# Kernel tuning notes

Hardware: AMD Instinct MI355X
Metric: run time of the kernel (lower is better)

## Reference

```python
import jax, jax.numpy as jnp
import numpy as np

NUM_ITERATIONS = 3


def squash(x, axis):
    # squared_norm/(1+squared_norm) * x / sqrt(squared_norm), as in the torch module
    sn = jnp.sum(x * x, axis=axis, keepdims=True)
    return sn / (1.0 + sn) * x / jnp.sqrt(sn)


def setup_inputs() -> dict:
    key = jax.random.key(0)
    k1, k2 = jax.random.split(key)
    batch, num_caps, num_route, in_ch, out_ch = 32, 32, 4608, 8, 16
    x = jax.random.normal(k1, (batch, num_route, in_ch), dtype=jnp.float32)
    route_weights = jax.random.normal(k2, (num_caps, num_route, in_ch, out_ch), dtype=jnp.float32)
    return {"x": x, "route_weights": route_weights}


def reference(x, route_weights):
    # U[b,c,r,1,o] = x[b,1,r,1,i] @ W[1,c,r,i,o]
    U = jnp.einsum("bri,crio->bcro", x, route_weights)[:, :, :, None, :]  # [b,c,r,1,o]
    B = jnp.zeros_like(U)
    V = None
    for _ in range(NUM_ITERATIONS):
        C = jax.nn.softmax(B, axis=1)                 # softmax over capsules
        S = jnp.sum(C * U, axis=2, keepdims=True)      # reduce over route nodes: [b,c,1,1,o]
        V = squash(S, axis=-1)
        B = B + U * V
    b, c = B.shape[0], B.shape[1]
    o = B.shape[-1]
    return V.reshape(b, c, o)
```

## Files before the change

### kernel.cpp

```cpp
#include <hip/hip_runtime.h>

#define BATCH 32
#define NCAPS 32
#define NR    4608
#define NI    8
#define NO    16
#define CSTR  200
#define MAXRB 36
#define NCH   256
#define L2E   1.44269504088896341f

typedef float f2 __attribute__((ext_vector_type(2)));
typedef _Float16 half4v __attribute__((ext_vector_type(4)));
typedef _Float16 half8v __attribute__((ext_vector_type(8)));

template<int RB>
__global__ __launch_bounds__(1024, 2) void caps_route_store(
    const float* __restrict__ x,
    const float* __restrict__ W,
    float* __restrict__ P,
    unsigned short* __restrict__ Uh)
{
    constexpr int NP = RB / 2;
    __shared__ __align__(16) float Ws[2][2][NCAPS * CSTR];
    __shared__ __align__(16) f2    xP[RB][8][2][NI];

    const int t  = threadIdx.x;
    const int om = (t & 3) | (((t >> 3) & 1) << 2);
    const int co = ((t >> 4) & 1) | (((t >> 2) & 1) << 1) | (((t >> 5) & 1) << 2);
    const int w  = t >> 6;
    const int oh = w & 1;
    const int bq = w >> 1;
    const int o  = oh * 8 + om;
    const int b0 = 4 * bq;
    const int r0 = blockIdx.x * RB;

    f2 acc[2][4];
#pragma unroll
    for (int p = 0; p < 2; ++p)
#pragma unroll
        for (int cl = 0; cl < 4; ++cl) acc[p][cl] = (f2)0.f;

    for (int s = t; s < RB * 16; s += 1024) {
        const int rr = s >> 4, bp = s & 15;
        const float* xp0 = &x[((size_t)(2 * bp + 0) * NR + r0 + rr) * NI];
        const float* xp1 = &x[((size_t)(2 * bp + 1) * NR + r0 + rr) * NI];
        const float4 a0 = *(const float4*)xp0;
        const float4 a1 = *(const float4*)(xp0 + 4);
        const float4 c0 = *(const float4*)xp1;
        const float4 c1 = *(const float4*)(xp1 + 4);
        f2* d = &xP[rr][bp >> 1][bp & 1][0];
        d[0] = f2{a0.x, c0.x}; d[1] = f2{a0.y, c0.y};
        d[2] = f2{a0.z, c0.z}; d[3] = f2{a0.w, c0.w};
        d[4] = f2{a1.x, c1.x}; d[5] = f2{a1.y, c1.y};
        d[6] = f2{a1.z, c1.z}; d[7] = f2{a1.w, c1.w};
    }

    const int c_st = t >> 5;
    const int sl   = (c_st >> 2) + 8 * (c_st & 3);
    const int part = t & 31;
    const int i_st = part >> 2;
    const int o0   = (part & 3) * 4;
    const int dst  = sl * CSTR + o0 * 12 + i_st;
    const float* wsrc = W + ((size_t)c_st * NR + r0) * (NI * NO) + part * 4;

    {
        const float4 s0 = *(const float4*)wsrc;
        const float4 s1 = *(const float4*)(wsrc + NI * NO);
        float* d0 = &Ws[0][0][dst];
        d0[0] = s0.x; d0[12] = s0.y; d0[24] = s0.z; d0[36] = s0.w;
        float* d1 = &Ws[0][1][dst];
        d1[0] = s1.x; d1[12] = s1.y; d1[24] = s1.z; d1[36] = s1.w;
    }
    float4 pfa = {}, pfb = {};
    if (NP > 1) {
        pfa = *(const float4*)(wsrc + 2 * NI * NO);
        pfb = *(const float4*)(wsrc + 3 * NI * NO);
    }
    __syncthreads();

    auto compute_store = [&](const float* wt, const f2* xv, int r) {
        f2 xq[2][NI];
#pragma unroll
        for (int i = 0; i < NI; ++i) { xq[0][i] = xv[i]; xq[1][i] = xv[NI + i]; }
        const float* wb = wt + co * CSTR + o * 12;
        f2 u[2][4];
#pragma unroll
        for (int cl = 0; cl < 4; ++cl) {
            const float* wp = wb + cl * (8 * CSTR);
            const float4 w0 = *(const float4*)wp;
            const float4 w1 = *(const float4*)(wp + 4);
#pragma unroll
            for (int p = 0; p < 2; ++p) {
                f2 u2 = xq[p][0] * w0.x;
                u2 += xq[p][1] * w0.y;
                u2 += xq[p][2] * w0.z;
                u2 += xq[p][3] * w0.w;
                u2 += xq[p][4] * w1.x;
                u2 += xq[p][5] * w1.y;
                u2 += xq[p][6] * w1.z;
                u2 += xq[p][7] * w1.w;
                u[p][cl] = u2;
                acc[p][cl] += u2;
            }
        }
        unsigned short* ub = Uh + (((size_t)r * BATCH + b0) * NO + o) * NCAPS + 4 * co;
#pragma unroll
        for (int bb = 0; bb < 4; ++bb) {
            const int p = bb >> 1, h = bb & 1;
            half4v hv;
            hv[0] = (_Float16)(h ? u[p][0].y : u[p][0].x);
            hv[1] = (_Float16)(h ? u[p][1].y : u[p][1].x);
            hv[2] = (_Float16)(h ? u[p][2].y : u[p][2].x);
            hv[3] = (_Float16)(h ? u[p][3].y : u[p][3].x);
            *(half4v*)(ub + (size_t)bb * (NO * NCAPS)) = hv;
        }
    };

#pragma unroll 1
    for (int rp = 0; rp < NP; ++rp) {
        const int cur = rp & 1;
        if (rp + 1 < NP) {
            float* d0 = &Ws[cur ^ 1][0][dst];
            d0[0] = pfa.x; d0[12] = pfa.y; d0[24] = pfa.z; d0[36] = pfa.w;
            float* d1 = &Ws[cur ^ 1][1][dst];
            d1[0] = pfb.x; d1[12] = pfb.y; d1[24] = pfb.z; d1[36] = pfb.w;
            if (rp + 2 < NP) {
                pfa = *(const float4*)(wsrc + (size_t)(2 * rp + 4) * (NI * NO));
                pfb = *(const float4*)(wsrc + (size_t)(2 * rp + 5) * (NI * NO));
            }
        }
        compute_store(&Ws[cur][0][0], &xP[2 * rp + 0][bq][0][0], r0 + 2 * rp + 0);
        compute_store(&Ws[cur][1][0], &xP[2 * rp + 1][bq][0][0], r0 + 2 * rp + 1);
        __syncthreads();
    }

#pragma unroll
    for (int bb = 0; bb < 4; ++bb) {
        const int p = bb >> 1, h = bb & 1;
        float* pout = P + (((size_t)blockIdx.x * BATCH + b0 + bb) * NO + o) * NCAPS + 4 * co;
        float4 v;
        v.x = (h ? acc[p][0].y : acc[p][0].x) * 0.03125f;
        v.y = (h ? acc[p][1].y : acc[p][1].x) * 0.03125f;
        v.z = (h ? acc[p][2].y : acc[p][2].x) * 0.03125f;
        v.w = (h ? acc[p][3].y : acc[p][3].x) * 0.03125f;
        *(float4*)pout = v;
    }
}

template<int RB>
__global__ __launch_bounds__(1024, 2) void caps_route_cached(
    const unsigned short* __restrict__ Uh,
    const float* __restrict__ A,
    float* __restrict__ P)
{
    const int t  = threadIdx.x;
    const int ch = t & 1;
    const int o  = (t >> 1) & 15;
    const int b  = t >> 5;
    const int r0 = blockIdx.x * RB;

    float a2[16];
#pragma unroll
    for (int cc = 0; cc < 16; ++cc)
        a2[cc] = A[(b * NCAPS + 16 * ch + cc) * NO + o] * L2E;
    float acc[16];
#pragma unroll
    for (int cc = 0; cc < 16; ++cc) acc[cc] = 0.f;

    const unsigned short* up =
        Uh + (((size_t)r0 * BATCH + b) * NO + o) * NCAPS + ch * 16;

#pragma unroll 1
    for (int rr = 0; rr < RB; ++rr) {
        const uint4 q0 = *(const uint4*)(up);
        const uint4 q1 = *(const uint4*)(up + 8);
        up += BATCH * NO * NCAPS;
        const half8v h0 = __builtin_bit_cast(half8v, q0);
        const half8v h1 = __builtin_bit_cast(half8v, q1);
        float u[16];
#pragma unroll
        for (int k = 0; k < 8; ++k) { u[k] = (float)h0[k]; u[8 + k] = (float)h1[k]; }
        float Z = 0.f;
        float tt[16];
#pragma unroll
        for (int cc = 0; cc < 16; ++cc) {
            const float uu = u[cc];
            const float ee = exp2f(uu * a2[cc]);
            Z += ee;
            tt[cc] = ee * uu;
        }
        Z += __shfl_xor(Z, 1);
        const float rz = __builtin_amdgcn_rcpf(Z);
#pragma unroll
        for (int cc = 0; cc < 16; ++cc)
            acc[cc] = fmaf(tt[cc], rz, acc[cc]);
    }

    float* pout = P + (((size_t)blockIdx.x * BATCH + b) * NO + o) * NCAPS + ch * 16;
#pragma unroll
    for (int q = 0; q < 4; ++q) {
        float4 v;
        v.x = acc[4 * q + 0]; v.y = acc[4 * q + 1];
        v.z = acc[4 * q + 2]; v.w = acc[4 * q + 3];
        *(float4*)(pout + 4 * q) = v;
    }
}

template<int RB, bool FIRST>
__global__ __launch_bounds__(1024, 2) void caps_route_fast(
    const float* __restrict__ x, const float* __restrict__ W,
    const float* __restrict__ A, float* __restrict__ P)
{
    constexpr int NP = RB / 2;
    __shared__ __align__(16) float Ws[2][2][NCAPS * CSTR];
    __shared__ __align__(16) f2    xP[RB][8][2][NI];

    const int t  = threadIdx.x;
    const int om = (t & 3) | (((t >> 3) & 1) << 2);
    const int co = ((t >> 4) & 1) | (((t >> 2) & 1) << 1) | (((t >> 5) & 1) << 2);
    const int w  = t >> 6;
    const int oh = w & 1;
    const int bq = w >> 1;
    const int o  = oh * 8 + om;
    const int b0 = 4 * bq;
    const int r0 = blockIdx.x * RB;

    f2 a2[2][4];
    if (!FIRST) {
#pragma unroll
        for (int p = 0; p < 2; ++p)
#pragma unroll
            for (int cl = 0; cl < 4; ++cl) {
                const int c = 4 * co + cl;
                a2[p][cl].x = A[((b0 + 2 * p + 0) * NCAPS + c) * NO + o] * L2E;
                a2[p][cl].y = A[((b0 + 2 * p + 1) * NCAPS + c) * NO + o] * L2E;
            }
    }
    f2 acc[2][4];
#pragma unroll
    for (int p = 0; p < 2; ++p)
#pragma unroll
        for (int cl = 0; cl < 4; ++cl) acc[p][cl] = (f2)0.f;

    for (int s = t; s < RB * 16; s += 1024) {
        const int rr = s >> 4, bp = s & 15;
        const float* xp0 = &x[((size_t)(2 * bp + 0) * NR + r0 + rr) * NI];
        const float* xp1 = &x[((size_t)(2 * bp + 1) * NR + r0 + rr) * NI];
        const float4 a0 = *(const float4*)xp0;
        const float4 a1 = *(const float4*)(xp0 + 4);
        const float4 c0 = *(const float4*)xp1;
        const float4 c1 = *(const float4*)(xp1 + 4);
        f2* d = &xP[rr][bp >> 1][bp & 1][0];
        d[0] = f2{a0.x, c0.x}; d[1] = f2{a0.y, c0.y};
        d[2] = f2{a0.z, c0.z}; d[3] = f2{a0.w, c0.w};
        d[4] = f2{a1.x, c1.x}; d[5] = f2{a1.y, c1.y};
        d[6] = f2{a1.z, c1.z}; d[7] = f2{a1.w, c1.w};
    }

    const int c_st = t >> 5;
    const int sl   = (c_st >> 2) + 8 * (c_st & 3);
    const int part = t & 31;
    const int i_st = part >> 2;
    const int o0   = (part & 3) * 4;
    const int dst  = sl * CSTR + o0 * 12 + i_st;
    const float* wsrc = W + ((size_t)c_st * NR + r0) * (NI * NO) + part * 4;

    {
        const float4 s0 = *(const float4*)wsrc;
        const float4 s1 = *(const float4*)(wsrc + NI * NO);
        float* d0 = &Ws[0][0][dst];
        d0[0] = s0.x; d0[12] = s0.y; d0[24] = s0.z; d0[36] = s0.w;
        float* d1 = &Ws[0][1][dst];
        d1[0] = s1.x; d1[12] = s1.y; d1[24] = s1.z; d1[36] = s1.w;
    }
    float4 pfa = {}, pfb = {};
    if (NP > 1) {
        pfa = *(const float4*)(wsrc + 2 * NI * NO);
        pfb = *(const float4*)(wsrc + 3 * NI * NO);
    }
    __syncthreads();

    auto compute_r = [&](const float* wt, const f2* xv) {
        f2 xq[2][NI];
#pragma unroll
        for (int i = 0; i < NI; ++i) { xq[0][i] = xv[i]; xq[1][i] = xv[NI + i]; }
        const float* wb = wt + co * CSTR + o * 12;
        if (FIRST) {
#pragma unroll
            for (int cl = 0; cl < 4; ++cl) {
                const float* wp = wb + cl * (8 * CSTR);
                const float4 w0 = *(const float4*)wp;
                const float4 w1 = *(const float4*)(wp + 4);
#pragma unroll
                for (int p = 0; p < 2; ++p) {
                    f2 u2 = xq[p][0] * w0.x;
                    u2 += xq[p][1] * w0.y;
                    u2 += xq[p][2] * w0.z;
                    u2 += xq[p][3] * w0.w;
                    u2 += xq[p][4] * w1.x;
                    u2 += xq[p][5] * w1.y;
                    u2 += xq[p][6] * w1.z;
                    u2 += xq[p][7] * w1.w;
                    acc[p][cl] += u2;
                }
            }
        } else {
            f2 tt[2][4];
            f2 Z0 = (f2)0.f, Z1 = (f2)0.f;
#pragma unroll
            for (int cl = 0; cl < 4; ++cl) {
                const float* wp = wb + cl * (8 * CSTR);
                const float4 w0 = *(const float4*)wp;
                const float4 w1 = *(const float4*)(wp + 4);
                f2 u0 = xq[0][0] * w0.x;
                u0 += xq[0][1] * w0.y;
                u0 += xq[0][2] * w0.z;
                u0 += xq[0][3] * w0.w;
                u0 += xq[0][4] * w1.x;
                u0 += xq[0][5] * w1.y;
                u0 += xq[0][6] * w1.z;
                u0 += xq[0][7] * w1.w;
                f2 u1 = xq[1][0] * w0.x;
                u1 += xq[1][1] * w0.y;
                u1 += xq[1][2] * w0.z;
                u1 += xq[1][3] * w0.w;
                u1 += xq[1][4] * w1.x;
                u1 += xq[1][5] * w1.y;
                u1 += xq[1][6] * w1.z;
                u1 += xq[1][7] * w1.w;
                const f2 l0 = u0 * a2[0][cl];
                const f2 l1 = u1 * a2[1][cl];
                f2 e0, e1;
                e0.x = exp2f(l0.x); e0.y = exp2f(l0.y);
                e1.x = exp2f(l1.x); e1.y = exp2f(l1.y);
                Z0 += e0; Z1 += e1;
                tt[0][cl] = e0 * u0;
                tt[1][cl] = e1 * u1;
            }
#pragma unroll
            for (int m = 0; m < 3; ++m) {
                const int msk = (m == 0) ? 4 : (m == 1) ? 16 : 32;
                Z0.x += __shfl_xor(Z0.x, msk); Z0.y += __shfl_xor(Z0.y, msk);
                Z1.x += __shfl_xor(Z1.x, msk); Z1.y += __shfl_xor(Z1.y, msk);
            }
            f2 rz0, rz1;
            rz0.x = __builtin_amdgcn_rcpf(Z0.x); rz0.y = __builtin_amdgcn_rcpf(Z0.y);
            rz1.x = __builtin_amdgcn_rcpf(Z1.x); rz1.y = __builtin_amdgcn_rcpf(Z1.y);
#pragma unroll
            for (int cl = 0; cl < 4; ++cl) {
                acc[0][cl] += tt[0][cl] * rz0;
                acc[1][cl] += tt[1][cl] * rz1;
            }
        }
    };

#pragma unroll 1
    for (int rp = 0; rp < NP; ++rp) {
        const int cur = rp & 1;
        if (rp + 1 < NP) {
            float* d0 = &Ws[cur ^ 1][0][dst];
            d0[0] = pfa.x; d0[12] = pfa.y; d0[24] = pfa.z; d0[36] = pfa.w;
            float* d1 = &Ws[cur ^ 1][1][dst];
            d1[0] = pfb.x; d1[12] = pfb.y; d1[24] = pfb.z; d1[36] = pfb.w;
            if (rp + 2 < NP) {
                pfa = *(const float4*)(wsrc + (size_t)(2 * rp + 4) * (NI * NO));
                pfb = *(const float4*)(wsrc + (size_t)(2 * rp + 5) * (NI * NO));
            }
        }
        compute_r(&Ws[cur][0][0], &xP[2 * rp + 0][bq][0][0]);
        compute_r(&Ws[cur][1][0], &xP[2 * rp + 1][bq][0][0]);
        __syncthreads();
    }

#pragma unroll
    for (int bb = 0; bb < 4; ++bb) {
        const int p = bb >> 1, h = bb & 1;
        float* pout = P + (((size_t)blockIdx.x * BATCH + b0 + bb) * NO + o) * NCAPS + 4 * co;
        float4 v;
        v.x = h ? acc[p][0].y : acc[p][0].x;
        v.y = h ? acc[p][1].y : acc[p][1].x;
        v.z = h ? acc[p][2].y : acc[p][2].x;
        v.w = h ? acc[p][3].y : acc[p][3].x;
        if (FIRST) { v.x *= 0.03125f; v.y *= 0.03125f; v.z *= 0.03125f; v.w *= 0.03125f; }
        *(float4*)pout = v;
    }
}

__global__ __launch_bounds__(256) void caps_partial(const float* __restrict__ P,
                                                    float* __restrict__ P2)
{
    const int tid = threadIdx.x;
    const int ct  = blockIdx.x & 15;
    const int rg  = blockIdx.x >> 4;
    const size_t col = (size_t)ct * 1024 + tid * 4;
    const float* p = P + (size_t)rg * 16 * 16384 + col;
    float4 s = {0.f, 0.f, 0.f, 0.f};
#pragma unroll
    for (int k = 0; k < 16; ++k) {
        const float4 v = *(const float4*)(p + (size_t)k * 16384);
        s.x += v.x; s.y += v.y; s.z += v.z; s.w += v.w;
    }
    *(float4*)(P2 + (size_t)rg * 16384 + col) = s;
}

__global__ void caps_reduce_squash(const float* __restrict__ P,
                                   float* __restrict__ A,
                                   float* __restrict__ out,
                                   int nchunk)
{
    __shared__ float sm[256];
    const int bc  = blockIdx.x;
    const int b   = bc >> 5;
    const int c   = bc & 31;
    const int tid = threadIdx.x;
    const int o = tid & 15;
    const int j = tid >> 4;
    float s = 0.f;
    for (int tch = j; tch < nchunk; tch += 16)
        s += P[(((size_t)tch * BATCH + b) * NO + o) * NCAPS + c];
    sm[tid] = s;
    __syncthreads();
    if (tid < 16) {
        float S = 0.f;
#pragma unroll
        for (int k = 0; k < 16; ++k) S += sm[tid + 16 * k];
        float sq = S * S;
#pragma unroll
        for (int d = 8; d >= 1; d >>= 1) sq += __shfl_xor(sq, d, 16);
        const float scale = sq / ((1.f + sq) * sqrtf(sq));
        const float V = S * scale;
        const int idx = bc * NO + tid;
        A[idx] += V;
        if (out) out[idx] = V;
    }
}

__global__ __launch_bounds__(512, 2) void caps_route_generic(
    const float* __restrict__ x, const float* __restrict__ W,
    const float* __restrict__ A, float* __restrict__ P, int rb)
{
    __shared__ __align__(16) float Ws[NCAPS * CSTR];
    __shared__ __align__(16) float xsT[NI * MAXRB * BATCH];

    const int t = threadIdx.x;
    const int b = t & 31;
    const int o = t >> 5;
    const int r0 = blockIdx.x * rb;
    const int rbs = rb * BATCH;

    float a2s[NCAPS];
#pragma unroll
    for (int c = 0; c < NCAPS; ++c)
        a2s[c] = A[(b * NCAPS + c) * NO + o] * L2E;
    float acc[NCAPS];
#pragma unroll
    for (int c = 0; c < NCAPS; ++c) acc[c] = 0.f;

    for (int s = t; s < rbs; s += 512) {
        const int rr = s >> 5, bb = s & 31;
        const float4 v0 = *(const float4*)&x[((size_t)bb * NR + r0 + rr) * NI];
        const float4 v1 = *(const float4*)&x[((size_t)bb * NR + r0 + rr) * NI + 4];
        const float tmp[8] = {v0.x, v0.y, v0.z, v0.w, v1.x, v1.y, v1.z, v1.w};
#pragma unroll
        for (int i = 0; i < NI; ++i) xsT[i * rbs + s] = tmp[i];
    }

    const int cs  = t >> 4;
    const int seg = t & 15;
    const int iw  = seg >> 1;
    const int ob  = (seg & 1) * 8;
    const float* wsrc = W + ((size_t)cs * NR + r0) * (NI * NO) + seg * 8;
    float4 pf0 = *(const float4*)wsrc;
    float4 pf1 = *(const float4*)(wsrc + 4);

    for (int rr = 0; rr < rb; ++rr) {
        __syncthreads();
        {
            const float tmp[8] = {pf0.x, pf0.y, pf0.z, pf0.w,
                                  pf1.x, pf1.y, pf1.z, pf1.w};
#pragma unroll
            for (int k = 0; k < 8; ++k)
                Ws[cs * CSTR + (ob + k) * 12 + iw] = tmp[k];
        }
        if (rr + 1 < rb) {
            wsrc += NI * NO;
            pf0 = *(const float4*)wsrc;
            pf1 = *(const float4*)(wsrc + 4);
        }
        __syncthreads();

        float xq[NI];
#pragma unroll
        for (int i = 0; i < NI; ++i) xq[i] = xsT[i * rbs + rr * 32 + b];

        float tt[NCAPS];
        float Z = 0.f;
        const float* bp2 = &Ws[o * 12];
#pragma unroll
        for (int c = 0; c < NCAPS; ++c) {
            const float* wp = bp2 + c * CSTR;
            const float4 w0 = *(const float4*)wp;
            const float4 w1 = *(const float4*)(wp + 4);
            float uu =      xq[0] * w0.x;
            uu = fmaf(xq[1], w0.y, uu);
            uu = fmaf(xq[2], w0.z, uu);
            uu = fmaf(xq[3], w0.w, uu);
            uu = fmaf(xq[4], w1.x, uu);
            uu = fmaf(xq[5], w1.y, uu);
            uu = fmaf(xq[6], w1.z, uu);
            uu = fmaf(xq[7], w1.w, uu);
            const float ee = exp2f(uu * a2s[c]);
            Z += ee;
            tt[c] = ee * uu;
        }
        const float rz = __builtin_amdgcn_rcpf(Z);
#pragma unroll
        for (int c = 0; c < NCAPS; ++c)
            acc[c] = fmaf(tt[c], rz, acc[c]);
    }

    float* pout = P + (((size_t)blockIdx.x * BATCH + b) * NO + o) * NCAPS;
#pragma unroll
    for (int q = 0; q < NCAPS / 4; ++q) {
        float4 v;
        v.x = acc[4 * q + 0]; v.y = acc[4 * q + 1];
        v.z = acc[4 * q + 2]; v.w = acc[4 * q + 3];
        *(float4*)(pout + 4 * q) = v;
    }
}

__global__ void caps_zero(float* __restrict__ p, int n)
{
    const int i = blockIdx.x * blockDim.x + threadIdx.x;
    if (i < n) p[i] = 0.f;
}

extern "C" void kernel_launch(void* const* d_in, const int* in_sizes, int n_in,
                              void* d_out, int out_size, void* d_ws, size_t ws_size,
                              hipStream_t stream)
{
    const float* x = (const float*)d_in[0];
    const float* W = (const float*)d_in[1];
    float* out = (float*)d_out;

    const size_t elem = (size_t)BATCH * NCAPS * NO;
    float* A  = (float*)d_ws;
    float* P  = A + elem;
    float* P2 = P + (size_t)NCH * elem;
    unsigned short* Uh = (unsigned short*)(P2 + 16 * elem);

    const size_t need_base = (size_t)(1 + NCH + 16) * elem * sizeof(float);
    const size_t need_u    = (size_t)NR * elem * sizeof(unsigned short);

    caps_zero<<<(int)((elem + 255) / 256), 256, 0, stream>>>(A, (int)elem);

    if (ws_size >= need_base + need_u) {
        caps_route_store<NR / NCH><<<NCH, 1024, 0, stream>>>(x, W, P, Uh);
        caps_partial<<<256, 256, 0, stream>>>(P, P2);
        caps_reduce_squash<<<BATCH * NCAPS, 256, 0, stream>>>(P2, A, nullptr, 16);
        caps_route_cached<NR / NCH><<<NCH, 1024, 0, stream>>>(Uh, A, P);
        caps_partial<<<256, 256, 0, stream>>>(P, P2);
        caps_reduce_squash<<<BATCH * NCAPS, 256, 0, stream>>>(P2, A, nullptr, 16);
        caps_route_cached<NR / NCH><<<NCH, 1024, 0, stream>>>(Uh, A, P);
        caps_partial<<<256, 256, 0, stream>>>(P, P2);
        caps_reduce_squash<<<BATCH * NCAPS, 256, 0, stream>>>(P2, A, out, 16);
    } else if (ws_size >= need_base) {
        caps_route_fast<NR / NCH, true><<<NCH, 1024, 0, stream>>>(x, W, A, P);
        caps_partial<<<256, 256, 0, stream>>>(P, P2);
        caps_reduce_squash<<<BATCH * NCAPS, 256, 0, stream>>>(P2, A, nullptr, 16);
        caps_route_fast<NR / NCH, false><<<NCH, 1024, 0, stream>>>(x, W, A, P);
        caps_partial<<<256, 256, 0, stream>>>(P, P2);
        caps_reduce_squash<<<BATCH * NCAPS, 256, 0, stream>>>(P2, A, nullptr, 16);
        caps_route_fast<NR / NCH, false><<<NCH, 1024, 0, stream>>>(x, W, A, P);
        caps_partial<<<256, 256, 0, stream>>>(P, P2);
        caps_reduce_squash<<<BATCH * NCAPS, 256, 0, stream>>>(P2, A, out, 16);
    } else {
        int nchunk = 128;
        while (nchunk > 32 &&
               (size_t)(nchunk + 1) * elem * sizeof(float) > ws_size)
            nchunk >>= 1;
        const int rb = NR / nchunk;
        for (int it = 0; it < 3; ++it) {
            caps_route_generic<<<nchunk, 512, 0, stream>>>(x, W, A, P, rb);
            caps_reduce_squash<<<BATCH * NCAPS, 256, 0, stream>>>(
                P, A, it == 2 ? out : nullptr, nchunk);
        }
    }
}
```

Baseline: 139.8 us.

## Split cached routing across twice the blocks with software-prefetched U loads

The cached routing kernel now gives each thread 8 capsules instead of 16. The batch is split across two blocks per route chunk, so the grid doubles to 512 blocks. The next route row's fp16 U vector is prefetched into registers before the current row is processed, to hide global-load latency. The softmax normaliser now needs a two-level cross-lane shuffle. The change adds parallelism and memory-level concurrency at the cost of more shuffles per element.

```diff
diff --git a/kernel.cpp b/kernel.cpp
--- a/kernel.cpp
+++ b/kernel.cpp
@@ -154,57 +154,59 @@
     const float* __restrict__ A,
     float* __restrict__ P)
 {
-    const int t  = threadIdx.x;
-    const int ch = t & 1;
-    const int o  = (t >> 1) & 15;
-    const int b  = t >> 5;
-    const int r0 = blockIdx.x * RB;
-
-    float a2[16];
-#pragma unroll
-    for (int cc = 0; cc < 16; ++cc)
-        a2[cc] = A[(b * NCAPS + 16 * ch + cc) * NO + o] * L2E;
-    float acc[16];
-#pragma unroll
-    for (int cc = 0; cc < 16; ++cc) acc[cc] = 0.f;
-
+    const int t     = threadIdx.x;
+    const int ch2   = t & 3;
+    const int o     = (t >> 2) & 15;
+    const int brel  = t >> 6;
+    const int chunk = blockIdx.x >> 1;
+    const int b     = 16 * (blockIdx.x & 1) + brel;
+    const int r0    = chunk * RB;
+
+    float a2[8];
+#pragma unroll
+    for (int cc = 0; cc < 8; ++cc)
+        a2[cc] = A[(b * NCAPS + 8 * ch2 + cc) * NO + o] * L2E;
+    float acc[8];
+#pragma unroll
+    for (int cc = 0; cc < 8; ++cc) acc[cc] = 0.f;
+
+    const size_t S = (size_t)BATCH * NO * NCAPS;
     const unsigned short* up =
-        Uh + (((size_t)r0 * BATCH + b) * NO + o) * NCAPS + ch * 16;
-
+        Uh + (((size_t)r0 * BATCH + b) * NO + o) * NCAPS + 8 * ch2;
+
+    uint4 q = *(const uint4*)up;
 #pragma unroll 1
     for (int rr = 0; rr < RB; ++rr) {
-        const uint4 q0 = *(const uint4*)(up);
-        const uint4 q1 = *(const uint4*)(up + 8);
-        up += BATCH * NO * NCAPS;
-        const half8v h0 = __builtin_bit_cast(half8v, q0);
-        const half8v h1 = __builtin_bit_cast(half8v, q1);
-        float u[16];
-#pragma unroll
-        for (int k = 0; k < 8; ++k) { u[k] = (float)h0[k]; u[8 + k] = (float)h1[k]; }
+        uint4 n = {};
+        if (rr + 1 < RB) n = *(const uint4*)(up + S);
+        up += S;
+
+        const half8v h = __builtin_bit_cast(half8v, q);
         float Z = 0.f;
-        float tt[16];
-#pragma unroll
-        for (int cc = 0; cc < 16; ++cc) {
-            const float uu = u[cc];
+        float tt[8];
+#pragma unroll
+        for (int cc = 0; cc < 8; ++cc) {
+            const float uu = (float)h[cc];
             const float ee = exp2f(uu * a2[cc]);
             Z += ee;
             tt[cc] = ee * uu;
         }
         Z += __shfl_xor(Z, 1);
+        Z += __shfl_xor(Z, 2);
         const float rz = __builtin_amdgcn_rcpf(Z);
 #pragma unroll
-        for (int cc = 0; cc < 16; ++cc)
+        for (int cc = 0; cc < 8; ++cc)
             acc[cc] = fmaf(tt[cc], rz, acc[cc]);
-    }
-
-    float* pout = P + (((size_t)blockIdx.x * BATCH + b) * NO + o) * NCAPS + ch * 16;
-#pragma unroll
-    for (int q = 0; q < 4; ++q) {
-        float4 v;
-        v.x = acc[4 * q + 0]; v.y = acc[4 * q + 1];
-        v.z = acc[4 * q + 2]; v.w = acc[4 * q + 3];
-        *(float4*)(pout + 4 * q) = v;
-    }
+
+        q = n;
+    }
+
+    float* pout = P + (((size_t)chunk * BATCH + b) * NO + o) * NCAPS + 8 * ch2;
+    float4 v0, v1;
+    v0.x = acc[0]; v0.y = acc[1]; v0.z = acc[2]; v0.w = acc[3];
+    v1.x = acc[4]; v1.y = acc[5]; v1.z = acc[6]; v1.w = acc[7];
+    *(float4*)pout = v0;
+    *(float4*)(pout + 4) = v1;
 }
 
 template<int RB, bool FIRST>
@@ -559,10 +561,10 @@
         caps_route_store<NR / NCH><<<NCH, 1024, 0, stream>>>(x, W, P, Uh);
         caps_partial<<<256, 256, 0, stream>>>(P, P2);
         caps_reduce_squash<<<BATCH * NCAPS, 256, 0, stream>>>(P2, A, nullptr, 16);
-        caps_route_cached<NR / NCH><<<NCH, 1024, 0, stream>>>(Uh, A, P);
+        caps_route_cached<NR / NCH><<<2 * NCH, 1024, 0, stream>>>(Uh, A, P);
         caps_partial<<<256, 256, 0, stream>>>(P, P2);
         caps_reduce_squash<<<BATCH * NCAPS, 256, 0, stream>>>(P2, A, nullptr, 16);
-        caps_route_cached<NR / NCH><<<NCH, 1024, 0, stream>>>(Uh, A, P);
+        caps_route_cached<NR / NCH><<<2 * NCH, 1024, 0, stream>>>(Uh, A, P);
         caps_partial<<<256, 256, 0, stream>>>(P, P2);
         caps_reduce_squash<<<BATCH * NCAPS, 256, 0, stream>>>(P2, A, out, 16);
     } else if (ws_size >= need_base) {
```

Result: faster. 132.3 us (-5.3%).
